# Kernel optimization log

Hardware: AMD Instinct MI355X
Metric: run time of the kernel (lower is better)

## Reference

```python
import jax, jax.numpy as jnp
import numpy as np

EPS = 1e-6
K = 1.0          # curvature parameter from init_kwargs
DIM = 2          # spatial dim hardcoded via default dim=2 in log/exponential
N = 500_000      # num vertices
E = 8_000_000    # num edges
M = 8            # message feature dim


def setup_inputs() -> dict:
    key = jax.random.key(0)
    k1, k2, k3, k4 = jax.random.split(key, 4)
    # vertices on hyperboloid: -x0^2 + |xs|^2 = -K  =>  x0 = sqrt(K + |xs|^2)
    xs = jax.random.normal(k1, (N, DIM), jnp.float32) * 0.5
    x0 = jnp.sqrt(K + jnp.sum(xs * xs, -1, keepdims=True))
    vertices = jnp.concatenate([x0, xs], -1)                      # [N, 3]
    src = jax.random.randint(k2, (E,), 0, N)
    off = jax.random.randint(k3, (E,), 1, N)                      # avoid self-loops
    dst = (src + off) % N
    edges = jnp.stack([src, dst], -1)                             # [E, 2] int
    messages = jax.random.normal(k4, (E, M), jnp.float32)         # [E, M]
    return {"vertices": vertices, "edges": edges, "messages": messages}


def _mip(x, y, w):
    # Minkowski inner product, keepdims=True: [.., 3] -> [.., 1]
    return jnp.sum(x * y * w, -1, keepdims=True)


def reference(vertices, edges, messages):
    w = jnp.concatenate([-jnp.ones(1), jnp.ones(DIM)]).astype(vertices.dtype)
    weights = jnp.mean(messages, -1, keepdims=True)               # [E, 1]
    x = vertices[edges[:, 0]]                                     # [E, 3] source
    y = vertices[edges[:, 1]]                                     # [E, 3] target
    # log map: log_x(y)
    t = _mip(x, y, w)                                             # [E, 1]
    v = y + x * t / K
    vnorm = jnp.sqrt(_mip(v, v, w) + EPS)
    dist = jnp.arccosh(-t / K)                                    # hyperboloid distance
    vectors = (v / vnorm) * dist * weights                        # [E, 3]
    # unsorted_segment_mean over source vertex (empty segments -> 0, as in TF)
    seg = edges[:, 0]
    sums = jax.ops.segment_sum(vectors, seg, num_segments=N)      # [N, 3]
    cnt = jax.ops.segment_sum(jnp.ones((E, 1), vertices.dtype), seg, num_segments=N)
    agg = jnp.where(cnt > 0, sums / jnp.maximum(cnt, 1.0), 0.0)   # [N, 3]
    # exponential map exp_vertices(agg)
    anorm = jnp.sqrt(_mip(agg, agg, w) + EPS)
    sqrtk = np.float32(np.sqrt(K))
    T = anorm / sqrtk
    return jnp.cosh(T) * vertices + sqrtk * jnp.sinh(T) * (agg / anorm)
```

## Files before the change

### kernel.cpp

```cpp
#include <hip/hip_runtime.h>

#define EPSF 1e-6f
#define VB 2048
#define VB_SHIFT 11
#define CHUNK 4096
#define NBMAX 256

__global__ __launch_bounds__(256) void pad_kernel(const float* __restrict__ v,
                                                  float4* __restrict__ v4, int N)
{
    int stride = gridDim.x * blockDim.x;
    for (int i = blockIdx.x * blockDim.x + threadIdx.x; i < N; i += stride) {
        size_t b = 3 * (size_t)i;
        v4[i] = make_float4(v[b], v[b + 1], v[b + 2], 0.f);
    }
}

__global__ __launch_bounds__(512) void count_kernel(const int2* __restrict__ edges,
                                                    int* __restrict__ counts,
                                                    int E, int nb)
{
    __shared__ int hist[NBMAX];
    int c = blockIdx.x;
    int base = c * CHUNK;
    int cnt = min(CHUNK, E - base);
    for (int i = threadIdx.x; i < nb; i += 512) hist[i] = 0;
    __syncthreads();
    for (int k = threadIdx.x; k < cnt; k += 512) {
        int src = edges[base + k].x;
        atomicAdd(&hist[src >> VB_SHIFT], 1);
    }
    __syncthreads();
    for (int i = threadIdx.x; i < nb; i += 512) counts[(size_t)c * nb + i] = hist[i];
}

__global__ __launch_bounds__(64) void relscan_kernel(int* __restrict__ counts,
                                                     int* __restrict__ totals,
                                                     int nb, int nchunk)
{
    int b = blockIdx.x;
    int lane = threadIdx.x;
    int running = 0;
    for (int cbase = 0; cbase < nchunk; cbase += 64) {
        int c = cbase + lane;
        int v = (c < nchunk) ? counts[(size_t)c * nb + b] : 0;
        int s = v;
        for (int d = 1; d < 64; d <<= 1) {
            int o = __shfl_up(s, d);
            if (lane >= d) s += o;
        }
        if (c < nchunk) counts[(size_t)c * nb + b] = running + (s - v);
        running += __shfl(s, 63);
    }
    if (lane == 0) totals[b] = running;
}

__global__ __launch_bounds__(64) void bstart_kernel(const int* __restrict__ totals,
                                                    int* __restrict__ bucketStart, int nb)
{
    if (threadIdx.x == 0 && blockIdx.x == 0) {
        int run = 0;
        for (int b = 0; b < nb; ++b) { bucketStart[b] = run; run += totals[b]; }
        bucketStart[nb] = run;
    }
}

__global__ __launch_bounds__(512) void scatter_kernel(const int2* __restrict__ edges,
    const float4* __restrict__ messages,
    const int* __restrict__ rel,
    const int* __restrict__ bucketStart,
    uint2* __restrict__ rec,
    int E, int nb)
{
    __shared__ unsigned int  s_pack[CHUNK];
    __shared__ float         s_w[CHUNK];
    __shared__ unsigned char s_b[CHUNK];
    __shared__ int hist[NBMAX], lstart[NBMAX], cursor[NBMAX], goff[NBMAX];

    int c = blockIdx.x;
    int base = c * CHUNK;
    int cnt = min(CHUNK, E - base);

    for (int i = threadIdx.x; i < nb; i += 512) hist[i] = 0;
    __syncthreads();

    int2 ed[8]; float wg[8];
#pragma unroll
    for (int j = 0; j < 8; ++j) {
        int k = threadIdx.x + j * 512;
        if (k < cnt) {
            int2 e2 = edges[base + k];
            float4 m0 = messages[2 * (size_t)(base + k)];
            float4 m1 = messages[2 * (size_t)(base + k) + 1];
            ed[j] = e2;
            wg[j] = (((m0.x + m0.y) + (m0.z + m0.w)) +
                     ((m1.x + m1.y) + (m1.z + m1.w))) * 0.125f;
            atomicAdd(&hist[e2.x >> VB_SHIFT], 1);
        }
    }
    __syncthreads();
    if (threadIdx.x == 0) {
        int run = 0;
        for (int b = 0; b < nb; ++b) { lstart[b] = run; cursor[b] = run; run += hist[b]; }
    }
    __syncthreads();
#pragma unroll
    for (int j = 0; j < 8; ++j) {
        int k = threadIdx.x + j * 512;
        if (k < cnt) {
            int b = ed[j].x >> VB_SHIFT;
            int pos = atomicAdd(&cursor[b], 1);
            s_pack[pos] = ((unsigned int)(ed[j].x & (VB - 1)) << 19) | (unsigned int)ed[j].y;
            s_w[pos]    = wg[j];
            s_b[pos]    = (unsigned char)b;
        }
    }
    for (int i = threadIdx.x; i < nb; i += 512)
        goff[i] = bucketStart[i] + rel[(size_t)c * nb + i];
    __syncthreads();
    for (int k = threadIdx.x; k < cnt; k += 512) {
        int b = s_b[k];
        int g = goff[b] + (k - lstart[b]);
        rec[g] = make_uint2(s_pack[k], __float_as_uint(s_w[k]));
    }
}

__device__ __forceinline__ void edge_math(const float4 xv, const float4 yv, float w,
                                          float& o0, float& o1, float& o2)
{
    float t  = xv.y * yv.y + xv.z * yv.z - xv.x * yv.x;
    float v0 = yv.x + xv.x * t;
    float v1 = yv.y + xv.y * t;
    float v2 = yv.z + xv.z * t;
    float vn = sqrtf(v1 * v1 + v2 * v2 - v0 * v0 + EPSF);
    float scale = acoshf(-t) * w / vn;
    o0 = v0 * scale; o1 = v1 * scale; o2 = v2 * scale;
}

__global__ __launch_bounds__(512, 8) void accum_kernel(
    const float4* __restrict__ vert4,
    const uint2*  __restrict__ rec,
    const int* __restrict__ bucketStart,
    float4* __restrict__ partial,
    int N, int nslice)
{
    __shared__ float acc[4][VB];
    int b = blockIdx.x / nslice;
    int s = blockIdx.x - b * nslice;
    for (int i = threadIdx.x; i < VB; i += 512) {
        acc[0][i] = 0.f; acc[1][i] = 0.f; acc[2][i] = 0.f; acc[3][i] = 0.f;
    }
    __syncthreads();
    int e0 = bucketStart[b], e1 = bucketStart[b + 1];
    int len = e1 - e0;
    int g0 = e0 + (int)((long long)len * s / nslice);
    int g1 = e0 + (int)((long long)len * (s + 1) / nslice);
    int vbase = b << VB_SHIFT;

    int base = g0;
    for (; base + 4 * 512 <= g1; base += 4 * 512) {
        int g = base + threadIdx.x;
        uint2 r0 = rec[g];
        uint2 r1 = rec[g + 512];
        uint2 r2 = rec[g + 1024];
        uint2 r3 = rec[g + 1536];
        int d0 = (int)(r0.x & 0x7FFFFu), l0 = (int)(r0.x >> 19);
        int d1 = (int)(r1.x & 0x7FFFFu), l1 = (int)(r1.x >> 19);
        int d2 = (int)(r2.x & 0x7FFFFu), l2 = (int)(r2.x >> 19);
        int d3 = (int)(r3.x & 0x7FFFFu), l3 = (int)(r3.x >> 19);
        float4 y0 = vert4[d0], y1 = vert4[d1], y2 = vert4[d2], y3 = vert4[d3];
        float4 x0 = vert4[vbase + l0], x1 = vert4[vbase + l1];
        float4 x2 = vert4[vbase + l2], x3 = vert4[vbase + l3];

        float a0, a1, a2;
        edge_math(x0, y0, __uint_as_float(r0.y), a0, a1, a2);
        atomicAdd(&acc[0][l0], a0); atomicAdd(&acc[1][l0], a1);
        atomicAdd(&acc[2][l0], a2); atomicAdd(&acc[3][l0], 1.0f);
        edge_math(x1, y1, __uint_as_float(r1.y), a0, a1, a2);
        atomicAdd(&acc[0][l1], a0); atomicAdd(&acc[1][l1], a1);
        atomicAdd(&acc[2][l1], a2); atomicAdd(&acc[3][l1], 1.0f);
        edge_math(x2, y2, __uint_as_float(r2.y), a0, a1, a2);
        atomicAdd(&acc[0][l2], a0); atomicAdd(&acc[1][l2], a1);
        atomicAdd(&acc[2][l2], a2); atomicAdd(&acc[3][l2], 1.0f);
        edge_math(x3, y3, __uint_as_float(r3.y), a0, a1, a2);
        atomicAdd(&acc[0][l3], a0); atomicAdd(&acc[1][l3], a1);
        atomicAdd(&acc[2][l3], a2); atomicAdd(&acc[3][l3], 1.0f);
    }
    for (int g = base + threadIdx.x; g < g1; g += 512) {
        uint2 r = rec[g];
        int dst = (int)(r.x & 0x7FFFFu);
        int sl  = (int)(r.x >> 19);
        float4 yv = vert4[dst];
        float4 xv = vert4[vbase + sl];
        float a0, a1, a2;
        edge_math(xv, yv, __uint_as_float(r.y), a0, a1, a2);
        atomicAdd(&acc[0][sl], a0); atomicAdd(&acc[1][sl], a1);
        atomicAdd(&acc[2][sl], a2); atomicAdd(&acc[3][sl], 1.0f);
    }
    __syncthreads();
    float4* pb = partial + (size_t)s * N;
    for (int i = threadIdx.x; i < VB; i += 512) {
        int v = vbase + i;
        if (v < N)
            pb[v] = make_float4(acc[0][i], acc[1][i], acc[2][i], acc[3][i]);
    }
}

__global__ __launch_bounds__(256) void final_kernel(const float* __restrict__ vertices,
    const float4* __restrict__ partial, float* __restrict__ out, int N, int nslice)
{
    int i = blockIdx.x * 256 + threadIdx.x;
    if (i >= N) return;
    float s0 = 0.f, s1 = 0.f, s2 = 0.f, sc = 0.f;
    for (int s = 0; s < nslice; ++s) {
        float4 a = partial[(size_t)s * N + i];
        s0 += a.x; s1 += a.y; s2 += a.z; sc += a.w;
    }
    float g0 = 0.f, g1 = 0.f, g2 = 0.f;
    if (sc > 0.f) { g0 = s0 / sc; g1 = s1 / sc; g2 = s2 / sc; }
    float an = sqrtf(g1 * g1 + g2 * g2 - g0 * g0 + EPSF);
    float ch = coshf(an);
    float sh = sinhf(an) / an;
    size_t bix = 3 * (size_t)i;
    out[bix + 0] = ch * vertices[bix + 0] + sh * g0;
    out[bix + 1] = ch * vertices[bix + 1] + sh * g1;
    out[bix + 2] = ch * vertices[bix + 2] + sh * g2;
}


__global__ __launch_bounds__(256) void zero_kernel(float4* __restrict__ acc, int n4)
{
    int stride = gridDim.x * blockDim.x;
    for (int i = blockIdx.x * blockDim.x + threadIdx.x; i < n4; i += stride)
        acc[i] = make_float4(0.f, 0.f, 0.f, 0.f);
}

__global__ __launch_bounds__(256) void edge_kernel_dev(const float* __restrict__ vertices,
    const int2* __restrict__ edges, const float4* __restrict__ messages,
    float* __restrict__ acc, int E)
{
    int stride = gridDim.x * blockDim.x;
    for (int e = blockIdx.x * blockDim.x + threadIdx.x; e < E; e += stride) {
        int2 ed = edges[e];
        float4 m0 = messages[2 * e];
        float4 m1 = messages[2 * e + 1];
        float wgt = (((m0.x + m0.y) + (m0.z + m0.w)) +
                     ((m1.x + m1.y) + (m1.z + m1.w))) * 0.125f;
        const float* xp = vertices + 3 * (size_t)ed.x;
        const float* yp = vertices + 3 * (size_t)ed.y;
        float4 xv = make_float4(xp[0], xp[1], xp[2], 0.f);
        float4 yv = make_float4(yp[0], yp[1], yp[2], 0.f);
        float a0, a1, a2;
        edge_math(xv, yv, wgt, a0, a1, a2);
        float* a = acc + 4 * (size_t)ed.x;
        atomicAdd(a + 0, a0);
        atomicAdd(a + 1, a1);
        atomicAdd(a + 2, a2);
        atomicAdd(a + 3, 1.0f);
    }
}

__global__ __launch_bounds__(256) void vertex_kernel_fb(const float* __restrict__ vertices,
    const float4* __restrict__ acc, float* __restrict__ out, int N)
{
    int i = blockIdx.x * blockDim.x + threadIdx.x;
    if (i >= N) return;
    float4 a = acc[i];
    float g0 = 0.f, g1 = 0.f, g2 = 0.f;
    if (a.w > 0.f) { g0 = a.x / a.w; g1 = a.y / a.w; g2 = a.z / a.w; }
    float an = sqrtf(g1 * g1 + g2 * g2 - g0 * g0 + EPSF);
    float ch = coshf(an);
    float sh = sinhf(an) / an;
    size_t bix = 3 * (size_t)i;
    out[bix + 0] = ch * vertices[bix + 0] + sh * g0;
    out[bix + 1] = ch * vertices[bix + 1] + sh * g1;
    out[bix + 2] = ch * vertices[bix + 2] + sh * g2;
}


extern "C" void kernel_launch(void* const* d_in, const int* in_sizes, int n_in,
                              void* d_out, int out_size, void* d_ws, size_t ws_size,
                              hipStream_t stream)
{
    const float*  vertices = (const float*)d_in[0];
    const int2*   edges    = (const int2*)d_in[1];
    const float4* messages = (const float4*)d_in[2];
    float* out = (float*)d_out;

    int N = in_sizes[0] / 3;
    int E = in_sizes[1] / 2;
    int nb = (N + VB - 1) / VB;
    int nchunk = (E + CHUNK - 1) / CHUNK;

    size_t off = 0;
    auto alloc = [&](size_t bytes) { size_t o = off; off = (off + bytes + 255) & ~255ull; return o; };
    size_t o_rec = alloc((size_t)E * 8);
    size_t o_cnt = alloc((size_t)nchunk * nb * 4);
    size_t o_tot = alloc((size_t)nb * 4);
    size_t o_bst = alloc((size_t)(nb + 1) * 4);
    size_t o_v4  = alloc((size_t)N * 16);
    size_t fixed = off;

    size_t par_bytes = (size_t)N * 16;

    int nslice = 0;
    if (fixed + 4 * par_bytes <= ws_size)      nslice = 4;
    else if (fixed + 2 * par_bytes <= ws_size) nslice = 2;

    if (nb <= NBMAX && (unsigned)N <= (1u << 19) && nslice > 0) {
        char* w = (char*)d_ws;
        uint2* rec      = (uint2*)(w + o_rec);
        int* counts     = (int*)(w + o_cnt);
        int* totals     = (int*)(w + o_tot);
        int* bstart     = (int*)(w + o_bst);
        float4* v4      = (float4*)(w + o_v4);
        float4* partial = (float4*)(w + fixed);

        pad_kernel<<<1024, 256, 0, stream>>>(vertices, v4, N);
        count_kernel<<<nchunk, 512, 0, stream>>>(edges, counts, E, nb);
        relscan_kernel<<<nb, 64, 0, stream>>>(counts, totals, nb, nchunk);
        bstart_kernel<<<1, 64, 0, stream>>>(totals, bstart, nb);
        scatter_kernel<<<nchunk, 512, 0, stream>>>(edges, messages, counts, bstart,
                                                   rec, E, nb);
        accum_kernel<<<nb * nslice, 512, 0, stream>>>(v4, rec, bstart,
                                                      partial, N, nslice);
        final_kernel<<<(N + 255) / 256, 256, 0, stream>>>(vertices, partial, out, N, nslice);
    } else {
        float* acc = (float*)d_ws;
        zero_kernel<<<4096, 256, 0, stream>>>((float4*)acc, N);
        edge_kernel_dev<<<4096, 256, 0, stream>>>(vertices, edges, messages, acc, E);
        vertex_kernel_fb<<<(N + 255) / 256, 256, 0, stream>>>(vertices, (const float4*)acc, out, N);
    }
}
```

Measured before the change: 323.2 us.

## Sub-bin edges by destination range, stage source vertices in LDS, atomic bin cursors

Edges are now binned by source block and also by a destination quarter of the vertex range, so records within each source bucket are grouped by destination. This should improve cache locality of the destination-vertex gathers in the accumulate kernel. The per-chunk count matrix and relative scan are replaced by a grid-strided global histogram and atomic per-bin global cursors. Source vertices for each block are preloaded into shared memory, which lowers occupancy (launch bounds go from 8 to 4 blocks per unit). Edge ordering inside bins becomes nondeterministic, so float accumulation order varies between runs.

Result: slower. 415.7 us (+28.6%).

```diff
diff --git a/kernel.cpp b/kernel.cpp
--- a/kernel.cpp
+++ b/kernel.cpp
@@ -3,8 +3,10 @@
 #define EPSF 1e-6f
 #define VB 2048
 #define VB_SHIFT 11
+#define NT 4
+#define TSHIFT 17
 #define CHUNK 4096
-#define NBMAX 256
+#define NBINS_PAD 1024
 
 __global__ __launch_bounds__(256) void pad_kernel(const float* __restrict__ v,
                                                   float4* __restrict__ v4, int N)
@@ -16,72 +18,63 @@
     }
 }
 
+__global__ __launch_bounds__(512) void zero_int_kernel(int* __restrict__ p, int n)
+{
+    int i = blockIdx.x * 512 + threadIdx.x;
+    if (i < n) p[i] = 0;
+}
+
 __global__ __launch_bounds__(512) void count_kernel(const int2* __restrict__ edges,
-                                                    int* __restrict__ counts,
-                                                    int E, int nb)
-{
-    __shared__ int hist[NBMAX];
+                                                    int* __restrict__ totals,
+                                                    int E, int nbins)
+{
+    __shared__ int hist[NBINS_PAD];
+    for (int i = threadIdx.x; i < NBINS_PAD; i += 512) hist[i] = 0;
+    __syncthreads();
+    int stride = gridDim.x * 512;
+    for (int k = blockIdx.x * 512 + threadIdx.x; k < E; k += stride) {
+        int2 e2 = edges[k];
+        int bin = (e2.x >> VB_SHIFT) * NT + (e2.y >> TSHIFT);
+        atomicAdd(&hist[bin], 1);
+    }
+    __syncthreads();
+    for (int i = threadIdx.x; i < nbins; i += 512)
+        if (hist[i]) atomicAdd(&totals[i], hist[i]);
+}
+
+__global__ __launch_bounds__(64) void bstart_kernel(const int* __restrict__ totals,
+                                                    int* __restrict__ binStart,
+                                                    int* __restrict__ gcursor,
+                                                    int* __restrict__ bucketStart,
+                                                    int nbins, int nb)
+{
+    if (threadIdx.x == 0 && blockIdx.x == 0) {
+        int run = 0;
+        for (int i = 0; i < nbins; ++i) {
+            binStart[i] = run; gcursor[i] = run; run += totals[i];
+        }
+        binStart[nbins] = run;
+        for (int b = 0; b <= nb; ++b) bucketStart[b] = binStart[min(b * NT, nbins)];
+    }
+}
+
+__global__ __launch_bounds__(512) void scatter_kernel(const int2* __restrict__ edges,
+    const float4* __restrict__ messages,
+    int* __restrict__ gcursor,
+    uint2* __restrict__ rec,
+    int E, int nbins)
+{
+    __shared__ uint2          s_rec[CHUNK];
+    __shared__ unsigned short s_bin[CHUNK];
+    __shared__ int hist[NBINS_PAD], lstart[NBINS_PAD];
+    __shared__ int cursor[NBINS_PAD], goff[NBINS_PAD];
+    __shared__ int sA[NBINS_PAD], sB[NBINS_PAD];
+
     int c = blockIdx.x;
     int base = c * CHUNK;
     int cnt = min(CHUNK, E - base);
-    for (int i = threadIdx.x; i < nb; i += 512) hist[i] = 0;
-    __syncthreads();
-    for (int k = threadIdx.x; k < cnt; k += 512) {
-        int src = edges[base + k].x;
-        atomicAdd(&hist[src >> VB_SHIFT], 1);
-    }
-    __syncthreads();
-    for (int i = threadIdx.x; i < nb; i += 512) counts[(size_t)c * nb + i] = hist[i];
-}
-
-__global__ __launch_bounds__(64) void relscan_kernel(int* __restrict__ counts,
-                                                     int* __restrict__ totals,
-                                                     int nb, int nchunk)
-{
-    int b = blockIdx.x;
-    int lane = threadIdx.x;
-    int running = 0;
-    for (int cbase = 0; cbase < nchunk; cbase += 64) {
-        int c = cbase + lane;
-        int v = (c < nchunk) ? counts[(size_t)c * nb + b] : 0;
-        int s = v;
-        for (int d = 1; d < 64; d <<= 1) {
-            int o = __shfl_up(s, d);
-            if (lane >= d) s += o;
-        }
-        if (c < nchunk) counts[(size_t)c * nb + b] = running + (s - v);
-        running += __shfl(s, 63);
-    }
-    if (lane == 0) totals[b] = running;
-}
-
-__global__ __launch_bounds__(64) void bstart_kernel(const int* __restrict__ totals,
-                                                    int* __restrict__ bucketStart, int nb)
-{
-    if (threadIdx.x == 0 && blockIdx.x == 0) {
-        int run = 0;
-        for (int b = 0; b < nb; ++b) { bucketStart[b] = run; run += totals[b]; }
-        bucketStart[nb] = run;
-    }
-}
-
-__global__ __launch_bounds__(512) void scatter_kernel(const int2* __restrict__ edges,
-    const float4* __restrict__ messages,
-    const int* __restrict__ rel,
-    const int* __restrict__ bucketStart,
-    uint2* __restrict__ rec,
-    int E, int nb)
-{
-    __shared__ unsigned int  s_pack[CHUNK];
-    __shared__ float         s_w[CHUNK];
-    __shared__ unsigned char s_b[CHUNK];
-    __shared__ int hist[NBMAX], lstart[NBMAX], cursor[NBMAX], goff[NBMAX];
-
-    int c = blockIdx.x;
-    int base = c * CHUNK;
-    int cnt = min(CHUNK, E - base);
-
-    for (int i = threadIdx.x; i < nb; i += 512) hist[i] = 0;
+
+    for (int i = threadIdx.x; i < NBINS_PAD; i += 512) hist[i] = 0;
     __syncthreads();
 
     int2 ed[8]; float wg[8];
@@ -95,33 +88,46 @@
             ed[j] = e2;
             wg[j] = (((m0.x + m0.y) + (m0.z + m0.w)) +
                      ((m1.x + m1.y) + (m1.z + m1.w))) * 0.125f;
-            atomicAdd(&hist[e2.x >> VB_SHIFT], 1);
+            atomicAdd(&hist[(e2.x >> VB_SHIFT) * NT + (e2.y >> TSHIFT)], 1);
         }
     }
     __syncthreads();
-    if (threadIdx.x == 0) {
-        int run = 0;
-        for (int b = 0; b < nb; ++b) { lstart[b] = run; cursor[b] = run; run += hist[b]; }
-    }
-    __syncthreads();
+
+    for (int i = threadIdx.x; i < NBINS_PAD; i += 512) sA[i] = hist[i];
+    __syncthreads();
+    int* src = sA; int* dst = sB;
+    for (int off = 1; off < NBINS_PAD; off <<= 1) {
+        for (int i = threadIdx.x; i < NBINS_PAD; i += 512)
+            dst[i] = src[i] + ((i >= off) ? src[i - off] : 0);
+        __syncthreads();
+        int* t = src; src = dst; dst = t;
+    }
+    for (int i = threadIdx.x; i < NBINS_PAD; i += 512) {
+        int ex = (i > 0) ? src[i - 1] : 0;
+        lstart[i] = ex; cursor[i] = ex;
+    }
+    __syncthreads();
+
 #pragma unroll
     for (int j = 0; j < 8; ++j) {
         int k = threadIdx.x + j * 512;
         if (k < cnt) {
-            int b = ed[j].x >> VB_SHIFT;
-            int pos = atomicAdd(&cursor[b], 1);
-            s_pack[pos] = ((unsigned int)(ed[j].x & (VB - 1)) << 19) | (unsigned int)ed[j].y;
-            s_w[pos]    = wg[j];
-            s_b[pos]    = (unsigned char)b;
+            int bin = (ed[j].x >> VB_SHIFT) * NT + (ed[j].y >> TSHIFT);
+            int pos = atomicAdd(&cursor[bin], 1);
+            s_rec[pos] = make_uint2(
+                ((unsigned int)(ed[j].x & (VB - 1)) << 19) | (unsigned int)ed[j].y,
+                __float_as_uint(wg[j]));
+            s_bin[pos] = (unsigned short)bin;
         }
     }
-    for (int i = threadIdx.x; i < nb; i += 512)
-        goff[i] = bucketStart[i] + rel[(size_t)c * nb + i];
+    for (int i = threadIdx.x; i < nbins; i += 512) {
+        int h = hist[i];
+        if (h) goff[i] = atomicAdd(&gcursor[i], h);
+    }
     __syncthreads();
     for (int k = threadIdx.x; k < cnt; k += 512) {
-        int b = s_b[k];
-        int g = goff[b] + (k - lstart[b]);
-        rec[g] = make_uint2(s_pack[k], __float_as_uint(s_w[k]));
+        int bin = s_bin[k];
+        rec[goff[bin] + (k - lstart[bin])] = s_rec[k];
     }
 }
 
@@ -137,25 +143,28 @@
     o0 = v0 * scale; o1 = v1 * scale; o2 = v2 * scale;
 }
 
-__global__ __launch_bounds__(512, 8) void accum_kernel(
+__global__ __launch_bounds__(512, 4) void accum_kernel(
     const float4* __restrict__ vert4,
     const uint2*  __restrict__ rec,
     const int* __restrict__ bucketStart,
     float4* __restrict__ partial,
     int N, int nslice)
 {
-    __shared__ float acc[4][VB];
+    __shared__ float  acc[4][VB];
+    __shared__ float4 s_x[VB];
     int b = blockIdx.x / nslice;
     int s = blockIdx.x - b * nslice;
+    int vbase = b << VB_SHIFT;
     for (int i = threadIdx.x; i < VB; i += 512) {
         acc[0][i] = 0.f; acc[1][i] = 0.f; acc[2][i] = 0.f; acc[3][i] = 0.f;
+        int idx = vbase + i;
+        s_x[i] = (idx < N) ? vert4[idx] : make_float4(0.f, 0.f, 0.f, 0.f);
     }
     __syncthreads();
     int e0 = bucketStart[b], e1 = bucketStart[b + 1];
     int len = e1 - e0;
     int g0 = e0 + (int)((long long)len * s / nslice);
     int g1 = e0 + (int)((long long)len * (s + 1) / nslice);
-    int vbase = b << VB_SHIFT;
 
     int base = g0;
     for (; base + 4 * 512 <= g1; base += 4 * 512) {
@@ -169,8 +178,7 @@
         int d2 = (int)(r2.x & 0x7FFFFu), l2 = (int)(r2.x >> 19);
         int d3 = (int)(r3.x & 0x7FFFFu), l3 = (int)(r3.x >> 19);
         float4 y0 = vert4[d0], y1 = vert4[d1], y2 = vert4[d2], y3 = vert4[d3];
-        float4 x0 = vert4[vbase + l0], x1 = vert4[vbase + l1];
-        float4 x2 = vert4[vbase + l2], x3 = vert4[vbase + l3];
+        float4 x0 = s_x[l0], x1 = s_x[l1], x2 = s_x[l2], x3 = s_x[l3];
 
         float a0, a1, a2;
         edge_math(x0, y0, __uint_as_float(r0.y), a0, a1, a2);
@@ -188,12 +196,11 @@
     }
     for (int g = base + threadIdx.x; g < g1; g += 512) {
         uint2 r = rec[g];
-        int dst = (int)(r.x & 0x7FFFFu);
-        int sl  = (int)(r.x >> 19);
-        float4 yv = vert4[dst];
-        float4 xv = vert4[vbase + sl];
+        int dsti = (int)(r.x & 0x7FFFFu);
+        int sl   = (int)(r.x >> 19);
+        float4 yv = vert4[dsti];
         float a0, a1, a2;
-        edge_math(xv, yv, __uint_as_float(r.y), a0, a1, a2);
+        edge_math(s_x[sl], yv, __uint_as_float(r.y), a0, a1, a2);
         atomicAdd(&acc[0][sl], a0); atomicAdd(&acc[1][sl], a1);
         atomicAdd(&acc[2][sl], a2); atomicAdd(&acc[3][sl], 1.0f);
     }
@@ -290,15 +297,17 @@
     int N = in_sizes[0] / 3;
     int E = in_sizes[1] / 2;
     int nb = (N + VB - 1) / VB;
+    int nbins = nb * NT;
     int nchunk = (E + CHUNK - 1) / CHUNK;
 
     size_t off = 0;
     auto alloc = [&](size_t bytes) { size_t o = off; off = (off + bytes + 255) & ~255ull; return o; };
-    size_t o_rec = alloc((size_t)E * 8);
-    size_t o_cnt = alloc((size_t)nchunk * nb * 4);
-    size_t o_tot = alloc((size_t)nb * 4);
-    size_t o_bst = alloc((size_t)(nb + 1) * 4);
-    size_t o_v4  = alloc((size_t)N * 16);
+    size_t o_rec  = alloc((size_t)E * 8);
+    size_t o_v4   = alloc((size_t)N * 16);
+    size_t o_tot  = alloc((size_t)nbins * 4);
+    size_t o_bins = alloc((size_t)(nbins + 1) * 4);
+    size_t o_gcur = alloc((size_t)nbins * 4);
+    size_t o_bkt  = alloc((size_t)(nb + 1) * 4);
     size_t fixed = off;
 
     size_t par_bytes = (size_t)N * 16;
@@ -307,23 +316,25 @@
     if (fixed + 4 * par_bytes <= ws_size)      nslice = 4;
     else if (fixed + 2 * par_bytes <= ws_size) nslice = 2;
 
-    if (nb <= NBMAX && (unsigned)N <= (1u << 19) && nslice > 0) {
+    bool ok = (nbins <= NBINS_PAD) && ((unsigned)N <= (1u << 19)) &&
+              ((size_t)N <= ((size_t)NT << TSHIFT)) && nslice > 0;
+
+    if (ok) {
         char* w = (char*)d_ws;
         uint2* rec      = (uint2*)(w + o_rec);
-        int* counts     = (int*)(w + o_cnt);
+        float4* v4      = (float4*)(w + o_v4);
         int* totals     = (int*)(w + o_tot);
-        int* bstart     = (int*)(w + o_bst);
-        float4* v4      = (float4*)(w + o_v4);
+        int* binStart   = (int*)(w + o_bins);
+        int* gcursor    = (int*)(w + o_gcur);
+        int* bktStart   = (int*)(w + o_bkt);
         float4* partial = (float4*)(w + fixed);
 
         pad_kernel<<<1024, 256, 0, stream>>>(vertices, v4, N);
-        count_kernel<<<nchunk, 512, 0, stream>>>(edges, counts, E, nb);
-        relscan_kernel<<<nb, 64, 0, stream>>>(counts, totals, nb, nchunk);
-        bstart_kernel<<<1, 64, 0, stream>>>(totals, bstart, nb);
-        scatter_kernel<<<nchunk, 512, 0, stream>>>(edges, messages, counts, bstart,
-                                                   rec, E, nb);
-        accum_kernel<<<nb * nslice, 512, 0, stream>>>(v4, rec, bstart,
-                                                      partial, N, nslice);
+        zero_int_kernel<<<(nbins + 511) / 512, 512, 0, stream>>>(totals, nbins);
+        count_kernel<<<256, 512, 0, stream>>>(edges, totals, E, nbins);
+        bstart_kernel<<<1, 64, 0, stream>>>(totals, binStart, gcursor, bktStart, nbins, nb);
+        scatter_kernel<<<nchunk, 512, 0, stream>>>(edges, messages, gcursor, rec, E, nbins);
+        accum_kernel<<<nb * nslice, 512, 0, stream>>>(v4, rec, bktStart, partial, N, nslice);
         final_kernel<<<(N + 255) / 256, 256, 0, stream>>>(vertices, partial, out, N, nslice);
     } else {
         float* acc = (float*)d_ws;
```
